# Performance work log

Hardware: AMD Instinct MI355X
Metric: run time of the kernel (lower is better)

Reference implementation:

```python
import jax, jax.numpy as jnp
import numpy as np

N = 10000          # nodes
E = 160000         # random edges (self-loops added in reference, as PyG does)
HEADS = 32
DIMS = [4, 128, 512, 1028]
NEG_SLOPE_ATT = 0.2    # GATv2Conv default negative_slope
NEG_SLOPE_ACT = 0.01   # torch.nn.LeakyReLU default


def setup_inputs() -> dict:
    key = jax.random.key(0)
    ks = jax.random.split(key, 32)
    inp = {}
    inp["x"] = jax.random.normal(ks[0], (N, DIMS[0]), dtype=jnp.float32)
    inp["edge_index"] = jax.random.randint(ks[1], (2, E), 0, N, dtype=jnp.int32)
    k = 2
    for l in range(3):
        fi, fo = DIMS[l], DIMS[l + 1]
        s_in = 1.0 / np.sqrt(fi)
        s_att = 1.0 / np.sqrt(fo)
        inp[f"W{l+1}l"] = (jax.random.normal(ks[k], (fi, HEADS * fo)) * s_in).astype(jnp.float32); k += 1
        inp[f"b{l+1}l"] = jnp.zeros((HEADS * fo,), jnp.float32)
        inp[f"W{l+1}r"] = (jax.random.normal(ks[k], (fi, HEADS * fo)) * s_in).astype(jnp.float32); k += 1
        inp[f"b{l+1}r"] = jnp.zeros((HEADS * fo,), jnp.float32)
        inp[f"att{l+1}"] = (jax.random.normal(ks[k], (HEADS, fo)) * s_att).astype(jnp.float32); k += 1
        inp[f"bias{l+1}"] = jnp.zeros((fo,), jnp.float32)
    return inp


def gatv2_layer(x, src, dst, Wl, bl, Wr, br, att, bias):
    # x: [N, fi]; src/dst: [E'] (self-loops included); att: [H, C]
    H, C = att.shape
    n = x.shape[0]
    xl = (x @ Wl + bl).reshape(n, H, C)  # source transform
    xr = (x @ Wr + br).reshape(n, H, C)  # target transform

    def per_head(args):
        xlh, xrh, ah = args  # [N,C], [N,C], [C]
        s = jax.nn.leaky_relu(xlh[src] + xrh[dst], NEG_SLOPE_ATT)  # [E',C]
        e = s @ ah  # [E'] attention logits
        m = jax.ops.segment_max(e, dst, num_segments=n)
        p = jnp.exp(e - m[dst])
        den = jax.ops.segment_sum(p, dst, num_segments=n)
        alpha = p / den[dst]  # edge-softmax per destination
        return jax.ops.segment_sum(alpha[:, None] * xlh[src], dst, num_segments=n)  # [N,C]

    # iterate heads sequentially to keep peak memory at O(E*C), not O(E*H*C)
    out = jax.lax.map(per_head, (jnp.moveaxis(xl, 1, 0), jnp.moveaxis(xr, 1, 0), att))  # [H,N,C]
    return out.mean(axis=0) + bias  # concat=False -> head mean


def reference(x, edge_index, W1l, b1l, W1r, b1r, att1, bias1,
              W2l, b2l, W2r, b2r, att2, bias2,
              W3l, b3l, W3r, b3r, att3, bias3):
    n = x.shape[0]
    loop = jnp.arange(n, dtype=edge_index.dtype)
    src = jnp.concatenate([edge_index[0], loop])
    dst = jnp.concatenate([edge_index[1], loop])
    h = gatv2_layer(x, src, dst, W1l, b1l, W1r, b1r, att1, bias1)
    h = jax.nn.leaky_relu(h, NEG_SLOPE_ACT)
    h = gatv2_layer(h, src, dst, W2l, b2l, W2r, b2r, att2, bias2)
    h = jax.nn.leaky_relu(h, NEG_SLOPE_ACT)
    h = gatv2_layer(h, src, dst, W3l, b3l, W3r, b3r, att3, bias3)
    return h
```

## Files before the change

### kernel.cpp

```cpp
#include <hip/hip_runtime.h>
#include <cstddef>
#include <cstdint>


#define HEADS 32
#define SLOPE_ATT 0.2f
#define SLOPE_ACT 0.01f

typedef __bf16 bf16_t;
typedef __bf16 bf16x8 __attribute__((ext_vector_type(8)));
typedef float f32x16 __attribute__((ext_vector_type(16)));

#define GLDS16(gp, lp)                                                        \
  __builtin_amdgcn_global_load_lds(                                           \
      (const __attribute__((address_space(1))) void*)(gp),                    \
      (__attribute__((address_space(3))) void*)(lp), 16, 0, 0)


__global__ __launch_bounds__(256) void init_counts_kernel(int* counts, int n) {
  int i = blockIdx.x * 256 + threadIdx.x;
  if (i < n) counts[i] = 1;
}

__global__ __launch_bounds__(256) void count_kernel(const int* __restrict__ dst, int* counts, int E) {
  int e = blockIdx.x * 256 + threadIdx.x;
  if (e < E) atomicAdd(&counts[dst[e]], 1);
}

__global__ __launch_bounds__(1024) void scan_kernel(const int* __restrict__ counts,
                                                    int* __restrict__ row_ptr,
                                                    int* __restrict__ cursor, int n) {
  __shared__ int sums[1024];
  int t = threadIdx.x;
  int per = (n + 1023) >> 10;
  int base = t * per;
  int s = 0;
  for (int i = 0; i < per; i++) { int idx = base + i; if (idx < n) s += counts[idx]; }
  sums[t] = s;
  __syncthreads();
  for (int off = 1; off < 1024; off <<= 1) {
    int v = (t >= off) ? sums[t - off] : 0;
    __syncthreads();
    sums[t] += v;
    __syncthreads();
  }
  int run = (t == 0) ? 0 : sums[t - 1];
  for (int i = 0; i < per; i++) {
    int idx = base + i;
    if (idx < n) { row_ptr[idx] = run; cursor[idx] = run; run += counts[idx]; }
  }
  if (t == 1023) row_ptr[n] = sums[1023];
}

__global__ __launch_bounds__(256) void scatter_edges_kernel(const int* __restrict__ ei, int* cursor,
                                                            int* col_src, int* col_dst, int E) {
  int e = blockIdx.x * 256 + threadIdx.x;
  if (e >= E) return;
  int src = ei[e], dst = ei[E + e];
  int pos = atomicAdd(&cursor[dst], 1);
  col_src[pos] = src;
  col_dst[pos] = dst;
}

__global__ __launch_bounds__(256) void scatter_loops_kernel(int* cursor, int* col_src, int* col_dst, int N) {
  int nid = blockIdx.x * 256 + threadIdx.x;
  if (nid >= N) return;
  int pos = atomicAdd(&cursor[nid], 1);
  col_src[pos] = nid;
  col_dst[pos] = nid;
}


__global__ __launch_bounds__(256) void cvt_pack_kernel(const float* __restrict__ X,
                                                       bf16_t* __restrict__ hi,
                                                       bf16_t* __restrict__ lo,
                                                       int M, int Mpad, int K) {
  int t = blockIdx.x * 256 + threadIdx.x;
  int kchunks = K >> 3;
  int total = Mpad * kchunks;
  if (t >= total) return;
  int kc = t % kchunks;
  int m = t / kchunks;
  int mt = m >> 7, ml = m & 127;
  size_t o = ((size_t)(mt * kchunks + kc)) * 1024 + (size_t)ml * 8;
  float v[8];
  if (m < M) {
    float4 a = *(const float4*)(X + (size_t)m * K + kc * 8);
    float4 b = *(const float4*)(X + (size_t)m * K + kc * 8 + 4);
    v[0] = a.x; v[1] = a.y; v[2] = a.z; v[3] = a.w;
    v[4] = b.x; v[5] = b.y; v[6] = b.z; v[7] = b.w;
  } else {
#pragma unroll
    for (int i = 0; i < 8; i++) v[i] = 0.f;
  }
  union { bf16_t h[8]; float4 f; } uh, ul;
#pragma unroll
  for (int i = 0; i < 8; i++) {
    bf16_t h = (bf16_t)v[i];
    uh.h[i] = h;
    ul.h[i] = (bf16_t)(v[i] - (float)h);
  }
  *(float4*)(hi + o) = uh.f;
  *(float4*)(lo + o) = ul.f;
}


__global__ __launch_bounds__(256) void pack_w_group_kernel(const float* __restrict__ Wl,
                                                           const float* __restrict__ Wr,
                                                           bf16_t* __restrict__ hL, bf16_t* __restrict__ lL,
                                                           bf16_t* __restrict__ hR, bf16_t* __restrict__ lR,
                                                           int K, int C, int Npad, int ldW,
                                                           int h0, int G) {
  int side = blockIdx.y;
  const float* W = side ? Wr : Wl;
  bf16_t* Hi = side ? hR : hL;
  bf16_t* Lo = side ? lR : lL;
  int kchunks = K >> 3;
  int perhead = Npad * kchunks;
  int t = blockIdx.x * 256 + threadIdx.x;
  if (t >= G * perhead) return;
  int g = t / perhead, rem = t % perhead;
  int n = rem % Npad, kc = rem / Npad;
  int nt = n >> 7, nl = n & 127;
  size_t o = (size_t)g * Npad * K + ((size_t)(nt * kchunks + kc)) * 1024 + (size_t)nl * 8;
  int col0 = (h0 + g) * C;
  union { bf16_t hh[8]; float4 f; } uh, ul;
#pragma unroll
  for (int kk = 0; kk < 8; kk++) {
    int k = kc * 8 + kk;
    float v = (n < C) ? W[(size_t)k * ldW + col0 + n] : 0.f;
    bf16_t hv = (bf16_t)v;
    uh.hh[kk] = hv;
    ul.hh[kk] = (bf16_t)(v - (float)hv);
  }
  *(float4*)(Hi + o) = uh.f;
  *(float4*)(Lo + o) = ul.f;
}


__global__ __launch_bounds__(256) void gemm_mfma_v6(const bf16_t* __restrict__ Xh,
                                                    const bf16_t* __restrict__ Xl,
                                                    const bf16_t* __restrict__ BhL,
                                                    const bf16_t* __restrict__ BlL,
                                                    const bf16_t* __restrict__ BhR,
                                                    const bf16_t* __restrict__ BlR,
                                                    size_t bHeadStride,
                                                    const float* __restrict__ bl,
                                                    const float* __restrict__ br,
                                                    float* __restrict__ outL,
                                                    float* __restrict__ outR,
                                                    size_t outHeadStride,
                                                    int M, int K, int C, int h0) {
  int gx = gridDim.x, gy = gridDim.y, gz = gridDim.z;
  int nwg = gx * gy * gz;
  int p = blockIdx.x + gx * (blockIdx.y + gy * blockIdx.z);
  int q = nwg >> 3, r = nwg & 7;
  int xcd = p & 7, slot = p >> 3;
  int lid = (xcd < r ? xcd * (q + 1) : r * (q + 1) + (xcd - r) * q) + slot;
  const int NY = 8;
  int xzsz = gx * gz;
  int fullr = gy / NY;
  int lidf = fullr * NY * xzsz;
  int rectbase, ny, rem;
  if (lid < lidf) {
    int rect = lid / (NY * xzsz);
    rem = lid - rect * (NY * xzsz);
    rectbase = rect * NY;
    ny = NY;
  } else {
    rem = lid - lidf;
    rectbase = fullr * NY;
    ny = gy - rectbase;
  }
  int xz = rem / ny;
  int yl = rem - xz * ny;
  int bx = xz % gx;
  int bz = xz / gx;
  int by = rectbase + yl;

  int g = bz >> 1, side = bz & 1;
  const bf16_t* Bh = (side ? BhR : BhL) + (size_t)g * bHeadStride;
  const bf16_t* Bl = (side ? BlR : BlL) + (size_t)g * bHeadStride;
  const float* bias = side ? br : bl;
  float* out = (side ? outR : outL) + (size_t)g * outHeadStride;
  int col0 = (h0 + g) * C;

  __shared__ __align__(16) bf16_t AsH[4 * 128 * 8];
  __shared__ __align__(16) bf16_t AsL[4 * 128 * 8];
  __shared__ __align__(16) bf16_t BsH[4 * 128 * 8];
  __shared__ __align__(16) bf16_t BsL[4 * 128 * 8];

  int tid = threadIdx.x;
  int wave = tid >> 6, lane = tid & 63;
  int l31 = lane & 31, lhalf = lane >> 5;
  int mt = by;
  int ntb = bx * 128;
  int m0 = mt * 128;
  int kchunks = K >> 3;

  const bf16_t* Ah = Xh + (size_t)mt * K * 128;
  const bf16_t* Al = Xl + (size_t)mt * K * 128;
  const bf16_t* Bhp = Bh + (size_t)bx * kchunks * 1024;
  const bf16_t* Blp = Bl + (size_t)bx * kchunks * 1024;

  auto* asH3 = (__attribute__((address_space(3))) bf16_t*)AsH;
  auto* asL3 = (__attribute__((address_space(3))) bf16_t*)AsL;
  auto* bsH3 = (__attribute__((address_space(3))) bf16_t*)BsH;
  auto* bsL3 = (__attribute__((address_space(3))) bf16_t*)BsL;

  f32x16 acc[4];
#pragma unroll
  for (int i = 0; i < 4; i++)
#pragma unroll
    for (int rr = 0; rr < 16; rr++) acc[i][rr] = 0.f;

  for (int k0 = 0; k0 < K; k0 += 32) {
    int kc0 = k0 >> 3;
#pragma unroll
    for (int rr = 0; rr < 2; rr++) {
      int idx = tid + 256 * rr;
      size_t off = ((size_t)(kc0 + (idx >> 7))) * 1024 + (size_t)(idx & 127) * 8;
      int li = idx * 8;
      GLDS16(Ah + off, asH3 + li);
      GLDS16(Al + off, asL3 + li);
      GLDS16(Bhp + off, bsH3 + li);
      GLDS16(Blp + off, bsL3 + li);
    }
    __syncthreads();

#pragma unroll
    for (int s = 0; s < 2; s++) {
      int c = s * 2 + lhalf;
      int abase = (c * 128 + wave * 32 + l31) * 8;
      bf16x8 ah = *(const bf16x8*)&AsH[abase];
      bf16x8 al = *(const bf16x8*)&AsL[abase];
#pragma unroll
      for (int nt = 0; nt < 4; nt++) {
        int bbase = (c * 128 + nt * 32 + l31) * 8;
        bf16x8 bh = *(const bf16x8*)&BsH[bbase];
        bf16x8 blo = *(const bf16x8*)&BsL[bbase];
        acc[nt] = __builtin_amdgcn_mfma_f32_32x32x16_bf16(ah, bh, acc[nt], 0, 0, 0);
        acc[nt] = __builtin_amdgcn_mfma_f32_32x32x16_bf16(ah, blo, acc[nt], 0, 0, 0);
        acc[nt] = __builtin_amdgcn_mfma_f32_32x32x16_bf16(al, bh, acc[nt], 0, 0, 0);
      }
    }
    __syncthreads();
  }

#pragma unroll
  for (int nt = 0; nt < 4; nt++) {
    int n = ntb + nt * 32 + l31;
    if (n >= C) continue;
    float bv = bias[col0 + n];
#pragma unroll
    for (int rr = 0; rr < 16; rr++) {
      int row = (rr & 3) + 8 * (rr >> 2) + 4 * lhalf;
      int m = m0 + wave * 32 + row;
      if (m < M) out[(size_t)m * C + n] = acc[nt][rr] + bv;
    }
  }
}


#define BM 128
#define BN 128
#define BK 16
#define LDA (BM + 4)
#define LDB (BN + 4)

__global__ __launch_bounds__(256) void gemm128(const float* __restrict__ X,
                                               const float* __restrict__ Wl,
                                               const float* __restrict__ Wr,
                                               const float* __restrict__ bl,
                                               const float* __restrict__ br,
                                               float* __restrict__ outL,
                                               float* __restrict__ outR,
                                               int M, int K, int C, int ldW, int col0) {
  const float* W = blockIdx.z ? Wr : Wl;
  const float* bias = blockIdx.z ? br : bl;
  float* out = blockIdx.z ? outR : outL;

  __shared__ __align__(16) float As[BK][LDA];
  __shared__ __align__(16) float Bs[BK][LDB];

  int t = threadIdx.x;
  int tx = t & 15, ty = t >> 4;
  int m0 = blockIdx.y * BM, n0 = blockIdx.x * BN;

  float acc00[4][4] = {}, acc01[4][4] = {}, acc10[4][4] = {}, acc11[4][4] = {};

  for (int k0 = 0; k0 < K; k0 += BK) {
    {
      int kk = (t & 3) * 4;
#pragma unroll
      for (int p = 0; p < 2; p++) {
        int row = (t >> 2) + p * 64;
        int m = m0 + row;
        float4 v = make_float4(0.f, 0.f, 0.f, 0.f);
        if (m < M && (k0 + kk) < K)
          v = *(const float4*)(X + (size_t)m * K + k0 + kk);
        As[kk + 0][row] = v.x; As[kk + 1][row] = v.y;
        As[kk + 2][row] = v.z; As[kk + 3][row] = v.w;
      }
    }
    {
      int kk = t >> 4;
#pragma unroll
      for (int qq = 0; qq < 2; qq++) {
        int cn = (t & 15) * 4 + qq * 64;
        int n = n0 + cn;
        float4 v = make_float4(0.f, 0.f, 0.f, 0.f);
        if ((k0 + kk) < K && n + 3 < C)
          v = *(const float4*)(W + (size_t)(k0 + kk) * ldW + col0 + n);
        *(float4*)&Bs[kk][cn] = v;
      }
    }
    __syncthreads();

    int kmax = min(BK, K - k0);
    for (int kk = 0; kk < kmax; kk++) {
      float4 a0 = *(const float4*)&As[kk][ty * 4];
      float4 a1 = *(const float4*)&As[kk][64 + ty * 4];
      float4 b0 = *(const float4*)&Bs[kk][tx * 4];
      float4 b1 = *(const float4*)&Bs[kk][64 + tx * 4];
      float af0[4] = {a0.x, a0.y, a0.z, a0.w};
      float af1[4] = {a1.x, a1.y, a1.z, a1.w};
      float bf0[4] = {b0.x, b0.y, b0.z, b0.w};
      float bf1[4] = {b1.x, b1.y, b1.z, b1.w};
#pragma unroll
      for (int i = 0; i < 4; i++)
#pragma unroll
        for (int j = 0; j < 4; j++) {
          acc00[i][j] += af0[i] * bf0[j];
          acc01[i][j] += af0[i] * bf1[j];
          acc10[i][j] += af1[i] * bf0[j];
          acc11[i][j] += af1[i] * bf1[j];
        }
    }
    __syncthreads();
  }

#pragma unroll
  for (int ma = 0; ma < 2; ma++) {
#pragma unroll
    for (int i = 0; i < 4; i++) {
      int m = m0 + ma * 64 + ty * 4 + i;
      if (m >= M) continue;
#pragma unroll
      for (int nb = 0; nb < 2; nb++) {
        int n = n0 + nb * 64 + tx * 4;
        float (*blk)[4] = (ma == 0) ? ((nb == 0) ? acc00 : acc01)
                                    : ((nb == 0) ? acc10 : acc11);
        if (n + 3 < C) {
          float4 bv = *(const float4*)(bias + col0 + n);
          float4 o = make_float4(blk[i][0] + bv.x, blk[i][1] + bv.y,
                                 blk[i][2] + bv.z, blk[i][3] + bv.w);
          *(float4*)(out + (size_t)m * C + n) = o;
        }
      }
    }
  }
}


template <int F4PT>
__global__ __launch_bounds__(256) void edge_fused_multi(const int* __restrict__ row_ptr,
                                                        const int* __restrict__ col_src,
                                                        const float* __restrict__ xl,
                                                        const float* __restrict__ xr,
                                                        int ld4, size_t hstride4,
                                                        const float* __restrict__ att,
                                                        float* __restrict__ acc,
                                                        int C, int head0, int G) {
  constexpr int ITER = (F4PT * 64 + 255) / 256;
  int node = blockIdx.x;
  int tid = threadIdx.x;
  int wave = tid >> 6, lane = tid & 63;
  int C4 = C >> 2;
  int s = row_ptr[node], t = row_ptr[node + 1];

  __shared__ __align__(16) float4 slab[4][F4PT * 64];
  __shared__ float mred[4], dred[4];

  float4 vtot[ITER];
#pragma unroll
  for (int it = 0; it < ITER; it++) vtot[it] = make_float4(0.f, 0.f, 0.f, 0.f);

  for (int g = 0; g < G; g++) {
    const float4* xlb = (const float4*)xl + (size_t)g * hstride4;
    const float4* xrp = (const float4*)xr + (size_t)g * hstride4 + (size_t)node * ld4;
    const float4* ap = (const float4*)(att + (size_t)g * C);

    float4 xr4[F4PT], a4[F4PT], o4[F4PT];
#pragma unroll
    for (int k = 0; k < F4PT; k++) {
      int c4 = k * 64 + lane;
      bool ok = (c4 < C4);
      xr4[k] = ok ? xrp[c4] : make_float4(0.f, 0.f, 0.f, 0.f);
      a4[k] = ok ? ap[c4] : make_float4(0.f, 0.f, 0.f, 0.f);
      o4[k] = make_float4(0.f, 0.f, 0.f, 0.f);
    }
    float m = -1e30f, den = 0.f;

    for (int j = s + wave; j < t; j += 4) {
      int src = col_src[j];
      const float4* xlp = xlb + (size_t)src * ld4;
      float4 x4[F4PT];
      float e = 0.f;
#pragma unroll
      for (int k = 0; k < F4PT; k++) {
        int c4 = k * 64 + lane;
        x4[k] = (c4 < C4) ? xlp[c4] : make_float4(0.f, 0.f, 0.f, 0.f);
        float v;
        v = x4[k].x + xr4[k].x; v = fmaxf(v, 0.f) + SLOPE_ATT * fminf(v, 0.f); e += a4[k].x * v;
        v = x4[k].y + xr4[k].y; v = fmaxf(v, 0.f) + SLOPE_ATT * fminf(v, 0.f); e += a4[k].y * v;
        v = x4[k].z + xr4[k].z; v = fmaxf(v, 0.f) + SLOPE_ATT * fminf(v, 0.f); e += a4[k].z * v;
        v = x4[k].w + xr4[k].w; v = fmaxf(v, 0.f) + SLOPE_ATT * fminf(v, 0.f); e += a4[k].w * v;
      }
#pragma unroll
      for (int off = 1; off < 64; off <<= 1) e += __shfl_xor(e, off, 64);

      if (e <= m) {
        float p = expf(e - m);
        den += p;
#pragma unroll
        for (int k = 0; k < F4PT; k++) {
          o4[k].x += p * x4[k].x; o4[k].y += p * x4[k].y;
          o4[k].z += p * x4[k].z; o4[k].w += p * x4[k].w;
        }
      } else {
        float scale = expf(m - e);
        den = den * scale + 1.f;
#pragma unroll
        for (int k = 0; k < F4PT; k++) {
          o4[k].x = o4[k].x * scale + x4[k].x; o4[k].y = o4[k].y * scale + x4[k].y;
          o4[k].z = o4[k].z * scale + x4[k].z; o4[k].w = o4[k].w * scale + x4[k].w;
        }
        m = e;
      }
    }

    if (lane == 0) { mred[wave] = m; dred[wave] = den; }
    __syncthreads();
    float M2 = fmaxf(fmaxf(mred[0], mred[1]), fmaxf(mred[2], mred[3]));
    float dtot = dred[0] * expf(mred[0] - M2) + dred[1] * expf(mred[1] - M2) +
                 dred[2] * expf(mred[2] - M2) + dred[3] * expf(mred[3] - M2);
    float f = expf(m - M2);
#pragma unroll
    for (int k = 0; k < F4PT; k++) {
      float4 w4 = make_float4(o4[k].x * f, o4[k].y * f, o4[k].z * f, o4[k].w * f);
      slab[wave][k * 64 + lane] = w4;
    }
    __syncthreads();
    float inv = 1.0f / dtot;
#pragma unroll
    for (int it = 0; it < ITER; it++) {
      int c4 = tid + it * 256;
      if (c4 < C4) {
        float4 s0 = slab[0][c4], s1 = slab[1][c4], s2 = slab[2][c4], s3 = slab[3][c4];
        vtot[it].x += ((s0.x + s1.x) + (s2.x + s3.x)) * inv;
        vtot[it].y += ((s0.y + s1.y) + (s2.y + s3.y)) * inv;
        vtot[it].z += ((s0.z + s1.z) + (s2.z + s3.z)) * inv;
        vtot[it].w += ((s0.w + s1.w) + (s2.w + s3.w)) * inv;
      }
    }
    __syncthreads();
  }

  float4* accp = (float4*)(acc + (size_t)node * C);
#pragma unroll
  for (int it = 0; it < ITER; it++) {
    int c4 = tid + it * 256;
    if (c4 < C4) {
      if (head0 == 0) {
        accp[c4] = vtot[it];
      } else {
        float4 prev = accp[c4];
        accp[c4] = make_float4(prev.x + vtot[it].x, prev.y + vtot[it].y,
                               prev.z + vtot[it].z, prev.w + vtot[it].w);
      }
    }
  }
}


__global__ __launch_bounds__(256) void finalize_kernel(const float* __restrict__ acc,
                                                       const float* __restrict__ bias,
                                                       float* __restrict__ out,
                                                       int total, int C, int apply_act) {
  int i = blockIdx.x * 256 + threadIdx.x;
  if (i >= total) return;
  int c = i % C;
  float v = acc[i] * (1.0f / 32.0f) + bias[c];
  if (apply_act) v = (v >= 0.f) ? v : SLOPE_ACT * v;
  out[i] = v;
}


static inline size_t align16(size_t x) { return (x + 15) & ~size_t(15); }

extern "C" void kernel_launch(void* const* d_in, const int* in_sizes, int n_in,
                              void* d_out, int out_size, void* d_ws, size_t ws_size,
                              hipStream_t stream) {
  const float* x0 = (const float*)d_in[0];
  const int* ei = (const int*)d_in[1];

  const int N = in_sizes[0] / 4;
  const int E = in_sizes[1] / 2;
  const int ETOT = E + N;
  const int MTILES = (N + 127) / 128;
  const int MPAD = MTILES * 128;

  struct LayerP { const float *Wl, *bl, *Wr, *br, *att, *bias; int fi, fo; };
  LayerP L[3] = {
      {(const float*)d_in[2],  (const float*)d_in[3],  (const float*)d_in[4],
       (const float*)d_in[5],  (const float*)d_in[6],  (const float*)d_in[7],  4, 128},
      {(const float*)d_in[8],  (const float*)d_in[9],  (const float*)d_in[10],
       (const float*)d_in[11], (const float*)d_in[12], (const float*)d_in[13], 128, 512},
      {(const float*)d_in[14], (const float*)d_in[15], (const float*)d_in[16],
       (const float*)d_in[17], (const float*)d_in[18], (const float*)d_in[19], 512, 1028},
  };

  char* w = (char*)d_ws;
  auto alloc = [&](size_t bytes) { char* p = w; w += align16(bytes); return p; };
  int* counts   = (int*)alloc((size_t)N * 4);
  int* row_ptr  = (int*)alloc((size_t)(N + 1) * 4);
  int* cursor   = (int*)alloc((size_t)N * 4);
  int* col_src  = (int*)alloc((size_t)ETOT * 4);
  int* col_dst  = (int*)alloc((size_t)ETOT * 4);
  float* xlh    = (float*)alloc((size_t)N * 2056 * 4);
  float* xrh    = (float*)alloc((size_t)N * 2056 * 4);
  float* h1     = (float*)alloc((size_t)N * 128 * 4);
  float* h2     = (float*)alloc((size_t)N * 512 * 4);
  float* acc12  = (float*)alloc((size_t)N * 512 * 4);
  bf16_t* xph   = (bf16_t*)alloc((size_t)MPAD * 512 * 2);
  bf16_t* xpl   = (bf16_t*)alloc((size_t)MPAD * 512 * 2);
  const size_t WPK3 = (size_t)2 * 1152 * 512;
  bf16_t* w3hL  = (bf16_t*)alloc(WPK3 * 2);
  bf16_t* w3lL  = (bf16_t*)alloc(WPK3 * 2);
  bf16_t* w3hR  = (bf16_t*)alloc(WPK3 * 2);
  bf16_t* w3lR  = (bf16_t*)alloc(WPK3 * 2);
  const size_t WPK2 = (size_t)HEADS * 512 * 128;
  bf16_t* w2hL  = (bf16_t*)alloc(WPK2 * 2);
  bf16_t* w2lL  = (bf16_t*)alloc(WPK2 * 2);
  bf16_t* w2hR  = (bf16_t*)alloc(WPK2 * 2);
  bf16_t* w2lR  = (bf16_t*)alloc(WPK2 * 2);

  init_counts_kernel<<<(N + 255) / 256, 256, 0, stream>>>(counts, N);
  count_kernel<<<(E + 255) / 256, 256, 0, stream>>>(ei + E, counts, E);
  scan_kernel<<<1, 1024, 0, stream>>>(counts, row_ptr, cursor, N);
  scatter_edges_kernel<<<(E + 255) / 256, 256, 0, stream>>>(ei, cursor, col_src, col_dst, E);
  scatter_loops_kernel<<<(N + 255) / 256, 256, 0, stream>>>(cursor, col_src, col_dst, N);

  {
    int C = 128;
    float* acc = acc12;
    for (int g = 0; g < 4; g++) {
      dim3 ggrid(8, MTILES, 2);
      gemm128<<<ggrid, 256, 0, stream>>>(x0, L[0].Wl, L[0].Wr, L[0].bl, L[0].br,
                                         xlh, xrh, N, 4, 1024, HEADS * C, g * 1024);
      edge_fused_multi<1><<<N, 256, 0, stream>>>(row_ptr, col_src, xlh, xrh,
                                                 256, (size_t)32,
                                                 L[0].att + (size_t)(g * 8) * C,
                                                 acc, C, g * 8, 8);
    }
    finalize_kernel<<<((size_t)N * C + 255) / 256, 256, 0, stream>>>(acc, L[0].bias, h1,
                                                                     N * C, C, 1);
  }

  {
    int fi = 128, C = 512, ldW = HEADS * C, Npadh = 512, G = 4;
    float* acc = acc12;
    size_t NC = (size_t)N * C;
    int total = MPAD * (fi >> 3);
    cvt_pack_kernel<<<(total + 255) / 256, 256, 0, stream>>>(h1, xph, xpl, N, MPAD, fi);
    int wtotal = HEADS * Npadh * (fi >> 3);
    dim3 wgrid((wtotal + 255) / 256, 2);
    pack_w_group_kernel<<<wgrid, 256, 0, stream>>>(L[1].Wl, L[1].Wr, w2hL, w2lL, w2hR, w2lR,
                                                   fi, C, Npadh, ldW, 0, HEADS);
    size_t hstride = (size_t)Npadh * fi;
    for (int h0 = 0; h0 < HEADS; h0 += G) {
      dim3 ggrid(Npadh / 128, MTILES, 2 * G);
      gemm_mfma_v6<<<ggrid, 256, 0, stream>>>(xph, xpl,
                                              w2hL + h0 * hstride, w2lL + h0 * hstride,
                                              w2hR + h0 * hstride, w2lR + h0 * hstride,
                                              hstride, L[1].bl, L[1].br,
                                              xlh, xrh, NC, N, fi, C, h0);
      edge_fused_multi<2><<<N, 256, 0, stream>>>(row_ptr, col_src, xlh, xrh,
                                                 C / 4, NC / 4,
                                                 L[1].att + (size_t)h0 * C,
                                                 acc, C, h0, G);
    }
    finalize_kernel<<<((size_t)N * C + 255) / 256, 256, 0, stream>>>(acc, L[1].bias, h2,
                                                                     N * C, C, 1);
  }

  {
    int fi = 512, C = 1028, ldW = HEADS * C, Npadh = 1152, G = 2;
    float* acc = (float*)d_out;
    size_t NC = (size_t)N * C;
    int total = MPAD * (fi >> 3);
    cvt_pack_kernel<<<(total + 255) / 256, 256, 0, stream>>>(h2, xph, xpl, N, MPAD, fi);
    size_t hstride = (size_t)Npadh * fi;
    for (int h0 = 0; h0 < HEADS; h0 += G) {
      int wtotal = G * Npadh * (fi >> 3);
      dim3 wgrid((wtotal + 255) / 256, 2);
      pack_w_group_kernel<<<wgrid, 256, 0, stream>>>(L[2].Wl, L[2].Wr, w3hL, w3lL, w3hR, w3lR,
                                                     fi, C, Npadh, ldW, h0, G);
      dim3 ggrid(Npadh / 128, MTILES, 2 * G);
      gemm_mfma_v6<<<ggrid, 256, 0, stream>>>(xph, xpl, w3hL, w3lL, w3hR, w3lR,
                                              hstride, L[2].bl, L[2].br,
                                              xlh, xrh, NC, N, fi, C, h0);
      edge_fused_multi<5><<<N, 256, 0, stream>>>(row_ptr, col_src, xlh, xrh,
                                                 C / 4, NC / 4,
                                                 L[2].att + (size_t)h0 * C,
                                                 acc, C, h0, G);
    }
    finalize_kernel<<<((size_t)N * C + 255) / 256, 256, 0, stream>>>(acc, L[2].bias, (float*)d_out,
                                                                     N * C, C, 0);
  }
}
```

Baseline: 9.539 ms.

## Parametrize edge kernel group width, stash gathered rows in LDS, use fast math

Makes the edge-softmax aggregation kernel generic over the lane-group width. Layer 1 (C=128, one float4 per lane) now uses 32-lane groups so 8 edges are processed per block instead of 4, halving idle lanes. For layer 3 (F4PT=5), gathered source rows go into shared memory instead of registers to cut register pressure and raise occupancy, at the cost of extra LDS traffic. It also switches to __expf, fmaf, and a fmax-based leaky ReLU, which may slightly change numerics.

After: 9.145 ms. -4.1%, faster.

```diff
diff --git a/kernel.cpp b/kernel.cpp
--- a/kernel.cpp
+++ b/kernel.cpp
@@ -363,7 +363,7 @@
 }
 
 
-template <int F4PT>
+template <int F4PT, int WIDTH>
 __global__ __launch_bounds__(256) void edge_fused_multi(const int* __restrict__ row_ptr,
                                                         const int* __restrict__ col_src,
                                                         const float* __restrict__ xl,
@@ -372,15 +372,18 @@
                                                         const float* __restrict__ att,
                                                         float* __restrict__ acc,
                                                         int C, int head0, int G) {
-  constexpr int ITER = (F4PT * 64 + 255) / 256;
+  constexpr int NG = 256 / WIDTH;
+  constexpr int ROW = F4PT * WIDTH;
+  constexpr int ITER = (ROW + 255) / 256;
+  constexpr bool STASH = (F4PT >= 3);
   int node = blockIdx.x;
   int tid = threadIdx.x;
-  int wave = tid >> 6, lane = tid & 63;
+  int grp = tid / WIDTH, lane = tid % WIDTH;
   int C4 = C >> 2;
   int s = row_ptr[node], t = row_ptr[node + 1];
 
-  __shared__ __align__(16) float4 slab[4][F4PT * 64];
-  __shared__ float mred[4], dred[4];
+  __shared__ __align__(16) float4 slab[NG][ROW];
+  __shared__ float mred[NG], dred[NG];
 
   float4 vtot[ITER];
 #pragma unroll
@@ -394,7 +397,7 @@
     float4 xr4[F4PT], a4[F4PT], o4[F4PT];
 #pragma unroll
     for (int k = 0; k < F4PT; k++) {
-      int c4 = k * 64 + lane;
+      int c4 = k * WIDTH + lane;
       bool ok = (c4 < C4);
       xr4[k] = ok ? xrp[c4] : make_float4(0.f, 0.f, 0.f, 0.f);
       a4[k] = ok ? ap[c4] : make_float4(0.f, 0.f, 0.f, 0.f);
@@ -402,66 +405,82 @@
     }
     float m = -1e30f, den = 0.f;
 
-    for (int j = s + wave; j < t; j += 4) {
+    for (int j = s + grp; j < t; j += NG) {
       int src = col_src[j];
       const float4* xlp = xlb + (size_t)src * ld4;
       float4 x4[F4PT];
       float e = 0.f;
 #pragma unroll
       for (int k = 0; k < F4PT; k++) {
-        int c4 = k * 64 + lane;
-        x4[k] = (c4 < C4) ? xlp[c4] : make_float4(0.f, 0.f, 0.f, 0.f);
+        int c4 = k * WIDTH + lane;
+        float4 xv = (c4 < C4) ? xlp[c4] : make_float4(0.f, 0.f, 0.f, 0.f);
+        if constexpr (STASH) slab[grp][k * WIDTH + lane] = xv;
+        else x4[k] = xv;
         float v;
-        v = x4[k].x + xr4[k].x; v = fmaxf(v, 0.f) + SLOPE_ATT * fminf(v, 0.f); e += a4[k].x * v;
-        v = x4[k].y + xr4[k].y; v = fmaxf(v, 0.f) + SLOPE_ATT * fminf(v, 0.f); e += a4[k].y * v;
-        v = x4[k].z + xr4[k].z; v = fmaxf(v, 0.f) + SLOPE_ATT * fminf(v, 0.f); e += a4[k].z * v;
-        v = x4[k].w + xr4[k].w; v = fmaxf(v, 0.f) + SLOPE_ATT * fminf(v, 0.f); e += a4[k].w * v;
-      }
-#pragma unroll
-      for (int off = 1; off < 64; off <<= 1) e += __shfl_xor(e, off, 64);
+        v = xv.x + xr4[k].x; v = fmaxf(v, SLOPE_ATT * v); e = fmaf(a4[k].x, v, e);
+        v = xv.y + xr4[k].y; v = fmaxf(v, SLOPE_ATT * v); e = fmaf(a4[k].y, v, e);
+        v = xv.z + xr4[k].z; v = fmaxf(v, SLOPE_ATT * v); e = fmaf(a4[k].z, v, e);
+        v = xv.w + xr4[k].w; v = fmaxf(v, SLOPE_ATT * v); e = fmaf(a4[k].w, v, e);
+      }
+#pragma unroll
+      for (int off = 1; off < WIDTH; off <<= 1) e += __shfl_xor(e, off, 64);
 
       if (e <= m) {
-        float p = expf(e - m);
+        float p = __expf(e - m);
         den += p;
 #pragma unroll
         for (int k = 0; k < F4PT; k++) {
-          o4[k].x += p * x4[k].x; o4[k].y += p * x4[k].y;
-          o4[k].z += p * x4[k].z; o4[k].w += p * x4[k].w;
+          float4 xv;
+          if constexpr (STASH) xv = slab[grp][k * WIDTH + lane];
+          else xv = x4[k];
+          o4[k].x = fmaf(p, xv.x, o4[k].x); o4[k].y = fmaf(p, xv.y, o4[k].y);
+          o4[k].z = fmaf(p, xv.z, o4[k].z); o4[k].w = fmaf(p, xv.w, o4[k].w);
         }
       } else {
-        float scale = expf(m - e);
-        den = den * scale + 1.f;
+        float sc = __expf(m - e);
+        den = fmaf(den, sc, 1.f);
 #pragma unroll
         for (int k = 0; k < F4PT; k++) {
-          o4[k].x = o4[k].x * scale + x4[k].x; o4[k].y = o4[k].y * scale + x4[k].y;
-          o4[k].z = o4[k].z * scale + x4[k].z; o4[k].w = o4[k].w * scale + x4[k].w;
+          float4 xv;
+          if constexpr (STASH) xv = slab[grp][k * WIDTH + lane];
+          else xv = x4[k];
+          o4[k].x = fmaf(o4[k].x, sc, xv.x); o4[k].y = fmaf(o4[k].y, sc, xv.y);
+          o4[k].z = fmaf(o4[k].z, sc, xv.z); o4[k].w = fmaf(o4[k].w, sc, xv.w);
         }
         m = e;
       }
     }
 
-    if (lane == 0) { mred[wave] = m; dred[wave] = den; }
-    __syncthreads();
-    float M2 = fmaxf(fmaxf(mred[0], mred[1]), fmaxf(mred[2], mred[3]));
-    float dtot = dred[0] * expf(mred[0] - M2) + dred[1] * expf(mred[1] - M2) +
-                 dred[2] * expf(mred[2] - M2) + dred[3] * expf(mred[3] - M2);
-    float f = expf(m - M2);
+    if (lane == 0) { mred[grp] = m; dred[grp] = den; }
+    __syncthreads();
+    float M2 = -1e30f;
+#pragma unroll
+    for (int i = 0; i < NG; i++) M2 = fmaxf(M2, mred[i]);
+    float dtot = 0.f;
+#pragma unroll
+    for (int i = 0; i < NG; i++) dtot += dred[i] * __expf(mred[i] - M2);
+    float f = __expf(m - M2);
 #pragma unroll
     for (int k = 0; k < F4PT; k++) {
       float4 w4 = make_float4(o4[k].x * f, o4[k].y * f, o4[k].z * f, o4[k].w * f);
-      slab[wave][k * 64 + lane] = w4;
+      slab[grp][k * WIDTH + lane] = w4;
     }
     __syncthreads();
     float inv = 1.0f / dtot;
 #pragma unroll
     for (int it = 0; it < ITER; it++) {
       int c4 = tid + it * 256;
-      if (c4 < C4) {
-        float4 s0 = slab[0][c4], s1 = slab[1][c4], s2 = slab[2][c4], s3 = slab[3][c4];
-        vtot[it].x += ((s0.x + s1.x) + (s2.x + s3.x)) * inv;
-        vtot[it].y += ((s0.y + s1.y) + (s2.y + s3.y)) * inv;
-        vtot[it].z += ((s0.z + s1.z) + (s2.z + s3.z)) * inv;
-        vtot[it].w += ((s0.w + s1.w) + (s2.w + s3.w)) * inv;
+      if (c4 < ROW && c4 < C4) {
+        float sx = 0.f, sy = 0.f, sz = 0.f, sw = 0.f;
+#pragma unroll
+        for (int i = 0; i < NG; i++) {
+          float4 sv = slab[i][c4];
+          sx += sv.x; sy += sv.y; sz += sv.z; sw += sv.w;
+        }
+        vtot[it].x = fmaf(sx, inv, vtot[it].x);
+        vtot[it].y = fmaf(sy, inv, vtot[it].y);
+        vtot[it].z = fmaf(sz, inv, vtot[it].z);
+        vtot[it].w = fmaf(sw, inv, vtot[it].w);
       }
     }
     __syncthreads();
@@ -471,7 +490,7 @@
 #pragma unroll
   for (int it = 0; it < ITER; it++) {
     int c4 = tid + it * 256;
-    if (c4 < C4) {
+    if (c4 < ROW && c4 < C4) {
       if (head0 == 0) {
         accp[c4] = vtot[it];
       } else {
@@ -492,7 +511,7 @@
   if (i >= total) return;
   int c = i % C;
   float v = acc[i] * (1.0f / 32.0f) + bias[c];
-  if (apply_act) v = (v >= 0.f) ? v : SLOPE_ACT * v;
+  if (apply_act) v = fmaxf(v, SLOPE_ACT * v);
   out[i] = v;
 }
 
@@ -559,10 +578,10 @@
       dim3 ggrid(8, MTILES, 2);
       gemm128<<<ggrid, 256, 0, stream>>>(x0, L[0].Wl, L[0].Wr, L[0].bl, L[0].br,
                                          xlh, xrh, N, 4, 1024, HEADS * C, g * 1024);
-      edge_fused_multi<1><<<N, 256, 0, stream>>>(row_ptr, col_src, xlh, xrh,
-                                                 256, (size_t)32,
-                                                 L[0].att + (size_t)(g * 8) * C,
-                                                 acc, C, g * 8, 8);
+      edge_fused_multi<1, 32><<<N, 256, 0, stream>>>(row_ptr, col_src, xlh, xrh,
+                                                     256, (size_t)32,
+                                                     L[0].att + (size_t)(g * 8) * C,
+                                                     acc, C, g * 8, 8);
     }
     finalize_kernel<<<((size_t)N * C + 255) / 256, 256, 0, stream>>>(acc, L[0].bias, h1,
                                                                      N * C, C, 1);
@@ -586,10 +605,10 @@
                                               w2hR + h0 * hstride, w2lR + h0 * hstride,
                                               hstride, L[1].bl, L[1].br,
                                               xlh, xrh, NC, N, fi, C, h0);
-      edge_fused_multi<2><<<N, 256, 0, stream>>>(row_ptr, col_src, xlh, xrh,
-                                                 C / 4, NC / 4,
-                                                 L[1].att + (size_t)h0 * C,
-                                                 acc, C, h0, G);
+      edge_fused_multi<2, 64><<<N, 256, 0, stream>>>(row_ptr, col_src, xlh, xrh,
+                                                     C / 4, NC / 4,
+                                                     L[1].att + (size_t)h0 * C,
+                                                     acc, C, h0, G);
     }
     finalize_kernel<<<((size_t)N * C + 255) / 256, 256, 0, stream>>>(acc, L[1].bias, h2,
                                                                      N * C, C, 1);
@@ -611,10 +630,10 @@
       gemm_mfma_v6<<<ggrid, 256, 0, stream>>>(xph, xpl, w3hL, w3lL, w3hR, w3lR,
                                               hstride, L[2].bl, L[2].br,
                                               xlh, xrh, NC, N, fi, C, h0);
-      edge_fused_multi<5><<<N, 256, 0, stream>>>(row_ptr, col_src, xlh, xrh,
-                                                 C / 4, NC / 4,
-                                                 L[2].att + (size_t)h0 * C,
-                                                 acc, C, h0, G);
+      edge_fused_multi<5, 64><<<N, 256, 0, stream>>>(row_ptr, col_src, xlh, xrh,
+                                                     C / 4, NC / 4,
+                                                     L[2].att + (size_t)h0 * C,
+                                                     acc, C, h0, G);
     }
     finalize_kernel<<<((size_t)N * C + 255) / 256, 256, 0, stream>>>(acc, L[2].bias, (float*)d_out,
                                                                      N * C, C, 0);
```
